# Kernel tuning notes

Hardware: AMD Instinct MI355X
Metric: run time of the kernel (lower is better)

Reference implementation:

```python
import jax, jax.numpy as jnp
import numpy as np
import math

SCALE = math.sqrt(256.0)

def setup_inputs() -> dict:
    key = jax.random.key(0)
    k1, k2, k3, k4, k5 = jax.random.split(key, 5)
    B, C, T, D = 8, 80, 2048, 256
    bound = 1.0 / math.sqrt(C)
    x = jax.random.normal(k1, (B, C, T), dtype=jnp.float32)
    Wk = jax.random.uniform(k2, (D, C), minval=-bound, maxval=bound, dtype=jnp.float32)
    bk = jax.random.uniform(k3, (D,), minval=-bound, maxval=bound, dtype=jnp.float32)
    Wq = jax.random.uniform(k4, (D, C), minval=-bound, maxval=bound, dtype=jnp.float32)
    bq = jax.random.uniform(k5, (D,), minval=-bound, maxval=bound, dtype=jnp.float32)
    return {"x": x, "Wk": Wk, "bk": bk, "Wq": Wq, "bq": bq}

def reference(x, Wk, bk, Wq, bq):
    # x: [B, C=80, T]; work in time-major layout [B, T, C]
    xt = jnp.swapaxes(x, 1, 2)                      # [B, T, C]
    K = xt @ Wk.T + bk                              # [B, T, 256]
    Q = xt @ Wq.T + bq                              # [B, T, 256]
    # softmax over last dim (dim=2 in torch) of K Q^T / sqrt(256)
    att = jax.nn.softmax(jnp.einsum('bid,bjd->bij', K, Q) / SCALE, axis=2)
    # original per-timestep loop is exactly att @ xt (values = raw input, no V proj)
    out = jnp.einsum('bij,bjc->bic', att, xt)       # [B, T, C]
    return jnp.swapaxes(out, 1, 2)                  # [B, C, T]
```

## Files before the change

kernel.cpp:

```cpp
#include <hip/hip_runtime.h>
#include <hip/hip_bf16.h>
#include <math.h>

typedef __bf16 bf16;
typedef __bf16 bf16x8 __attribute__((ext_vector_type(8)));
typedef float  f32x4  __attribute__((ext_vector_type(4)));
typedef float  f32x16 __attribute__((ext_vector_type(16)));
typedef uint32_t u32x4 __attribute__((ext_vector_type(4)));

#define MFMA16(a, b, c) __builtin_amdgcn_mfma_f32_16x16x32_bf16((a), (b), (c), 0, 0, 0)
#define MFMA32(a, b, c) __builtin_amdgcn_mfma_f32_32x32x16_bf16((a), (b), (c), 0, 0, 0)

typedef const uint32_t __attribute__((address_space(1)))* gq_t;
typedef uint32_t __attribute__((address_space(3)))* lq_t;

constexpr int B_ = 8, C_ = 80, T_ = 2048, D_ = 256;
constexpr int NS = 8;
constexpr float SCALE_INV = 1.0f / 16.0f;
constexpr float LOG2E_16 = 0.090169989f;

static __device__ inline uint32_t pkbf(float lo, float hi) {
  bf16 l = (bf16)lo, h = (bf16)hi;
  uint16_t lb = __builtin_bit_cast(uint16_t, l), hb = __builtin_bit_cast(uint16_t, h);
  return (uint32_t)lb | ((uint32_t)hb << 16);
}

__global__ __launch_bounds__(256) void proj_kernel(
    const float* __restrict__ x,
    const float* __restrict__ Wk,
    const float* __restrict__ bk,
    const float* __restrict__ Wq,
    const float* __restrict__ bq,
    bf16* __restrict__ Kb,
    bf16* __restrict__ Qb,
    bf16* __restrict__ xbf)
{
  const int t0   = blockIdx.x * 32;
  const int b    = blockIdx.y;
  const int tid  = threadIdx.x;
  const int w    = tid >> 6;
  const int lane = tid & 63;
  const int h    = lane >> 4;
  const int lr   = lane & 15;

  const float* xb = x + (size_t)b * C_ * T_;

  {
    bf16* ob = xbf + (size_t)b * C_ * T_;
    #pragma unroll
    for (int q = 0; q < 10; ++q) {
      int idx = q * 256 + tid;
      int c = idx >> 5, tt = idx & 31;
      ob[c * T_ + t0 + tt] = (bf16)xb[c * T_ + t0 + tt];
    }
  }

  bf16x8 afrag[2][3];
  #pragma unroll
  for (int ib = 0; ib < 2; ++ib) {
    int t = t0 + ib * 16 + lr;
    #pragma unroll
    for (int ks = 0; ks < 3; ++ks) {
      bf16x8 v;
      #pragma unroll
      for (int e = 0; e < 8; ++e) {
        int c = ks * 32 + h * 8 + e;
        float val;
        if (c < 80)       val = xb[c * T_ + t];
        else if (c == 80) val = 1.0f;
        else              val = 0.0f;
        v[e] = (bf16)val;
      }
      afrag[ib][ks] = v;
    }
  }

  const int nb0 = w * 4;
  #pragma unroll
  for (int mat = 0; mat < 2; ++mat) {
    const float* W    = mat ? Wq : Wk;
    const float* bias = mat ? bq : bk;
    bf16* outp        = mat ? Qb : Kb;

    f32x4 acc[2][4];
    #pragma unroll
    for (int ib = 0; ib < 2; ++ib)
      #pragma unroll
      for (int nb = 0; nb < 4; ++nb)
        acc[ib][nb] = f32x4{0.f, 0.f, 0.f, 0.f};

    #pragma unroll
    for (int nb = 0; nb < 4; ++nb) {
      int d = (nb0 + nb) * 16 + lr;
      #pragma unroll
      for (int ks = 0; ks < 3; ++ks) {
        bf16x8 bv;
        #pragma unroll
        for (int e = 0; e < 8; ++e) {
          int c = ks * 32 + h * 8 + e;
          float val;
          if (c < 80)       val = W[d * C_ + c];
          else if (c == 80) val = bias[d];
          else              val = 0.0f;
          bv[e] = (bf16)val;
        }
        #pragma unroll
        for (int ib = 0; ib < 2; ++ib)
          acc[ib][nb] = MFMA16(afrag[ib][ks], bv, acc[ib][nb]);
      }
    }

    #pragma unroll
    for (int ib = 0; ib < 2; ++ib)
      #pragma unroll
      for (int nb = 0; nb < 4; ++nb) {
        int d = (nb0 + nb) * 16 + lr;
        #pragma unroll
        for (int r = 0; r < 4; ++r) {
          int t = t0 + ib * 16 + h * 4 + r;
          outp[(size_t)(b * T_ + t) * D_ + d] = (bf16)acc[ib][nb][r];
        }
      }
  }
}

__global__ __launch_bounds__(256, 2) void attn_kernel(
    const bf16* __restrict__ Kb,
    const bf16* __restrict__ Qb,
    const bf16* __restrict__ xbf,
    float* __restrict__ Opart,
    float* __restrict__ mpart,
    float* __restrict__ lpart)
{
  constexpr int BN = 32, NT = T_ / BN;
  constexpr int JT_PER = NT / NS;
  __shared__ bf16 qlds[2][BN * D_];

  const int flat = blockIdx.x;
  const int b    = flat & 7;
  const int rem  = flat >> 3;
  const int it   = rem & 15;
  const int s    = rem >> 4;
  const int i0   = it * 128;

  const int tid  = threadIdx.x;
  const int w    = tid >> 6;
  const int lane = tid & 63;
  const int il   = lane & 31;
  const int hi   = lane >> 5;
  const int iw   = i0 + w * 32;

  const bf16* Kbase = Kb  + (size_t)b * T_ * D_;
  const bf16* Qbase = Qb  + (size_t)b * T_ * D_;
  const bf16* Vbase = xbf + (size_t)b * C_ * T_;

  bf16x8 kf[16];
  {
    const bf16* kp = Kbase + (size_t)(iw + il) * D_ + hi * 8;
    #pragma unroll
    for (int ks = 0; ks < 16; ++ks)
      kf[ks] = *reinterpret_cast<const bf16x8*>(kp + ks * 16);
  }

  f32x16 oacc[3];
  #pragma unroll
  for (int cb = 0; cb < 3; ++cb)
    #pragma unroll
    for (int r = 0; r < 16; ++r) oacc[cb][r] = 0.f;
  float m_run = -INFINITY, l_run = 0.f;

  auto stage = [&](int jt, int buf) {
    #pragma unroll
    for (int q = 0; q < 4; ++q) {
      int f = tid + 256 * q;
      int j = f >> 5, c = f & 31;
      const bf16* src = Qbase + (size_t)(jt * BN + j) * D_ + ((c ^ j) << 3);
      __builtin_amdgcn_global_load_lds((gq_t)src,
          (lq_t)&qlds[buf][(q * 256 + w * 64) * 8], 16, 0, 0);
    }
  };

  const int jt0 = s * JT_PER, jtend = jt0 + JT_PER;

  stage(jt0, 0);
  asm volatile("s_waitcnt vmcnt(0)" ::: "memory");
  __syncthreads();

  int cur = 0;
  for (int jt = jt0; jt < jtend; ++jt, cur ^= 1) {
    if (jt + 1 < jtend) stage(jt + 1, cur ^ 1);

    bf16x8 vf[3][2];
    #pragma unroll
    for (int cb = 0; cb < 3; ++cb)
      #pragma unroll
      for (int kj = 0; kj < 2; ++kj)
        vf[cb][kj] = *reinterpret_cast<const bf16x8*>(
            Vbase + (size_t)(cb * 32 + il) * T_ + jt * BN + hi * 8 + kj * 16);

    f32x16 sacc;
    #pragma unroll
    for (int r = 0; r < 16; ++r) sacc[r] = 0.f;
    __builtin_amdgcn_s_setprio(1);
    #pragma unroll
    for (int ks = 0; ks < 16; ++ks) {
      bf16x8 qa = *reinterpret_cast<const bf16x8*>(
          &qlds[cur][il * 256 + (((hi + 2 * ks) ^ il) << 3)]);
      sacc = MFMA32(qa, kf[ks], sacc);
    }
    __builtin_amdgcn_s_setprio(0);

    float p16[16];
    #pragma unroll
    for (int r = 0; r < 16; ++r) p16[r] = sacc[r];
    float mx = p16[0];
    #pragma unroll
    for (int r = 1; r < 16; ++r) mx = fmaxf(mx, p16[r]);
    mx = fmaxf(mx, __shfl_xor(mx, 32));

    if (!__all(mx <= m_run + 48.f)) {
      float mnew  = fmaxf(m_run, mx);
      float alpha = exp2f((m_run - mnew) * LOG2E_16);
      m_run = mnew;
      l_run *= alpha;
      #pragma unroll
      for (int cb = 0; cb < 3; ++cb)
        #pragma unroll
        for (int r = 0; r < 16; ++r) oacc[cb][r] *= alpha;
    }
    float rs = 0.f;
    #pragma unroll
    for (int r = 0; r < 16; ++r) {
      p16[r] = exp2f((p16[r] - m_run) * LOG2E_16);
      rs += p16[r];
    }
    rs += __shfl_xor(rs, 32);
    l_run += rs;

    uint32_t a0 = pkbf(p16[0],  p16[1]),  a1 = pkbf(p16[2],  p16[3]);
    uint32_t c0 = pkbf(p16[4],  p16[5]),  c1 = pkbf(p16[6],  p16[7]);
    uint32_t a2 = pkbf(p16[8],  p16[9]),  a3 = pkbf(p16[10], p16[11]);
    uint32_t c2 = pkbf(p16[12], p16[13]), c3 = pkbf(p16[14], p16[15]);
    uint32_t a0s = __shfl_xor(a0, 32), a1s = __shfl_xor(a1, 32);
    uint32_t c0s = __shfl_xor(c0, 32), c1s = __shfl_xor(c1, 32);
    uint32_t a2s = __shfl_xor(a2, 32), a3s = __shfl_xor(a3, 32);
    uint32_t c2s = __shfl_xor(c2, 32), c3s = __shfl_xor(c3, 32);
    const bool h = (hi != 0);
    u32x4 pb0 = { h ? c0s : a0, h ? c1s : a1, h ? c0 : a0s, h ? c1 : a1s };
    u32x4 pb1 = { h ? c2s : a2, h ? c3s : a3, h ? c2 : a2s, h ? c3 : a3s };
    bf16x8 pbf0 = __builtin_bit_cast(bf16x8, pb0);
    bf16x8 pbf1 = __builtin_bit_cast(bf16x8, pb1);

    __builtin_amdgcn_s_setprio(1);
    #pragma unroll
    for (int cb = 0; cb < 3; ++cb) {
      oacc[cb] = MFMA32(vf[cb][0], pbf0, oacc[cb]);
      oacc[cb] = MFMA32(vf[cb][1], pbf1, oacc[cb]);
    }
    __builtin_amdgcn_s_setprio(0);

    asm volatile("s_waitcnt vmcnt(0)" ::: "memory");
    __syncthreads();
  }

  float* ob = Opart + (size_t)(s * B_ + b) * C_ * T_;
  #pragma unroll
  for (int cb = 0; cb < 3; ++cb)
    #pragma unroll
    for (int r = 0; r < 16; ++r) {
      if (cb < 2 || r < 8) {
        int c = cb * 32 + (r & 3) + 8 * (r >> 2) + 4 * hi;
        ob[(size_t)c * T_ + iw + il] = oacc[cb][r];
      }
    }
  if (lane < 32) {
    mpart[(size_t)(s * B_ + b) * T_ + iw + il] = m_run;
    lpart[(size_t)(s * B_ + b) * T_ + iw + il] = l_run;
  }
}

__global__ __launch_bounds__(256) void merge_kernel(
    const float* __restrict__ Opart,
    const float* __restrict__ mpart,
    const float* __restrict__ lpart,
    float* __restrict__ out)
{
  const int b    = blockIdx.y;
  const int tid  = threadIdx.x;
  const int w    = tid >> 6;
  const int lane = tid & 63;
  const int t    = blockIdx.x * 64 + lane;

  float m[NS];
  float mmax = -INFINITY;
  #pragma unroll
  for (int s2 = 0; s2 < NS; ++s2) {
    m[s2] = mpart[(size_t)(s2 * B_ + b) * T_ + t];
    mmax = fmaxf(mmax, m[s2]);
  }
  float e[NS];
  float lsum = 0.f;
  #pragma unroll
  for (int s2 = 0; s2 < NS; ++s2) {
    e[s2] = exp2f((m[s2] - mmax) * LOG2E_16);
    lsum += e[s2] * lpart[(size_t)(s2 * B_ + b) * T_ + t];
  }
  const float inv = 1.0f / lsum;

  const int c0 = w * 20;
  for (int c = c0; c < c0 + 20; ++c) {
    float acc = 0.f;
    #pragma unroll
    for (int s2 = 0; s2 < NS; ++s2)
      acc += Opart[((size_t)(s2 * B_ + b) * C_ + c) * T_ + t] * e[s2];
    out[((size_t)b * C_ + c) * T_ + t] = acc * inv;
  }
}

extern "C" void kernel_launch(void* const* d_in, const int* in_sizes, int n_in,
                              void* d_out, int out_size, void* d_ws, size_t ws_size,
                              hipStream_t stream) {
  (void)in_sizes; (void)n_in; (void)out_size; (void)ws_size;
  const float* x  = (const float*)d_in[0];
  const float* Wk = (const float*)d_in[1];
  const float* bk = (const float*)d_in[2];
  const float* Wq = (const float*)d_in[3];
  const float* bq = (const float*)d_in[4];
  float* out = (float*)d_out;

  char* ws = (char*)d_ws;
  const size_t MB = 1024 * 1024;
  bf16*  Kb    = (bf16*)(ws);
  bf16*  Qb    = (bf16*)(ws + 8 * MB);
  bf16*  xbf   = (bf16*)(ws + 16 * MB);
  float* Opart = (float*)(ws + 19 * MB);
  float* mpart = (float*)(ws + 61 * MB);
  float* lpart = (float*)(ws + 62 * MB);

  dim3 blk(256);
  dim3 g1(T_ / 32, B_);
  proj_kernel<<<g1, blk, 0, stream>>>(x, Wk, bk, Wq, bq, Kb, Qb, xbf);
  attn_kernel<<<dim3(16 * NS * B_), blk, 0, stream>>>(Kb, Qb, xbf, Opart, mpart, lpart);
  dim3 g3(T_ / 64, B_);
  merge_kernel<<<g3, blk, 0, stream>>>(Opart, mpart, lpart, out);
}
```

Before: 76.61 us.

## Software-pipeline QK^T of next tile with softmax/PV and halve KV splits

Restructures the attention inner loop into a two-stage pipeline. The Q·K MFMAs and V loads for tile t+1 are issued before the softmax and P·V of tile t, with double-buffered score accumulators and V fragments, and LDS staging runs two tiles ahead. This is meant to hide the latency of the exp/shuffle softmax section behind matrix work. It also cuts the number of sequence splits from 8 to 4, which halves the partial outputs the merge kernel must read, and shrinks the workspace offsets to match. The cost is higher register pressure and half as many blocks for parallelism.

```diff
diff --git a/kernel.cpp b/kernel.cpp
--- a/kernel.cpp
+++ b/kernel.cpp
@@ -15,8 +15,7 @@
 typedef uint32_t __attribute__((address_space(3)))* lq_t;
 
 constexpr int B_ = 8, C_ = 80, T_ = 2048, D_ = 256;
-constexpr int NS = 8;
-constexpr float SCALE_INV = 1.0f / 16.0f;
+constexpr int NS = 4;
 constexpr float LOG2E_16 = 0.090169989f;
 
 static __device__ inline uint32_t pkbf(float lo, float hi) {
@@ -180,36 +179,29 @@
     }
   };
 
-  const int jt0 = s * JT_PER, jtend = jt0 + JT_PER;
-
-  stage(jt0, 0);
-  asm volatile("s_waitcnt vmcnt(0)" ::: "memory");
-  __syncthreads();
-
-  int cur = 0;
-  for (int jt = jt0; jt < jtend; ++jt, cur ^= 1) {
-    if (jt + 1 < jtend) stage(jt + 1, cur ^ 1);
-
-    bf16x8 vf[3][2];
+  auto vload = [&](int jt, bf16x8 (&vf)[3][2]) {
     #pragma unroll
     for (int cb = 0; cb < 3; ++cb)
       #pragma unroll
       for (int kj = 0; kj < 2; ++kj)
         vf[cb][kj] = *reinterpret_cast<const bf16x8*>(
             Vbase + (size_t)(cb * 32 + il) * T_ + jt * BN + hi * 8 + kj * 16);
-
-    f32x16 sacc;
-    #pragma unroll
-    for (int r = 0; r < 16; ++r) sacc[r] = 0.f;
+  };
+
+  auto qkt = [&](int buf, f32x16& sc) {
+    #pragma unroll
+    for (int r = 0; r < 16; ++r) sc[r] = 0.f;
     __builtin_amdgcn_s_setprio(1);
     #pragma unroll
     for (int ks = 0; ks < 16; ++ks) {
       bf16x8 qa = *reinterpret_cast<const bf16x8*>(
-          &qlds[cur][il * 256 + (((hi + 2 * ks) ^ il) << 3)]);
-      sacc = MFMA32(qa, kf[ks], sacc);
+          &qlds[buf][il * 256 + (((hi + 2 * ks) ^ il) << 3)]);
+      sc = MFMA32(qa, kf[ks], sc);
     }
     __builtin_amdgcn_s_setprio(0);
-
+  };
+
+  auto smax_pv = [&](f32x16& sacc, bf16x8 (&vf)[3][2]) {
     float p16[16];
     #pragma unroll
     for (int r = 0; r < 16; ++r) p16[r] = sacc[r];
@@ -245,9 +237,9 @@
     uint32_t c0s = __shfl_xor(c0, 32), c1s = __shfl_xor(c1, 32);
     uint32_t a2s = __shfl_xor(a2, 32), a3s = __shfl_xor(a3, 32);
     uint32_t c2s = __shfl_xor(c2, 32), c3s = __shfl_xor(c3, 32);
-    const bool h = (hi != 0);
-    u32x4 pb0 = { h ? c0s : a0, h ? c1s : a1, h ? c0 : a0s, h ? c1 : a1s };
-    u32x4 pb1 = { h ? c2s : a2, h ? c3s : a3, h ? c2 : a2s, h ? c3 : a3s };
+    const bool hh = (hi != 0);
+    u32x4 pb0 = { hh ? c0s : a0, hh ? c1s : a1, hh ? c0 : a0s, hh ? c1 : a1s };
+    u32x4 pb1 = { hh ? c2s : a2, hh ? c3s : a3, hh ? c2 : a2s, hh ? c3 : a3s };
     bf16x8 pbf0 = __builtin_bit_cast(bf16x8, pb0);
     bf16x8 pbf1 = __builtin_bit_cast(bf16x8, pb1);
 
@@ -258,9 +250,36 @@
       oacc[cb] = MFMA32(vf[cb][1], pbf1, oacc[cb]);
     }
     __builtin_amdgcn_s_setprio(0);
-
+  };
+
+  const int jt0 = s * JT_PER, jtend = jt0 + JT_PER;
+
+  f32x16 saccA, saccB;
+  bf16x8 vfA[3][2], vfB[3][2];
+
+  stage(jt0, 0);
+  asm volatile("s_waitcnt vmcnt(0)" ::: "memory");
+  __syncthreads();
+  vload(jt0, vfA);
+  qkt(0, saccA);
+  stage(jt0 + 1, 1);
+
+  auto body = [&](int t, f32x16& sp, f32x16& sc,
+                  bf16x8 (&va)[3][2], bf16x8 (&vb)[3][2], int par) {
     asm volatile("s_waitcnt vmcnt(0)" ::: "memory");
     __syncthreads();
+    if (t + 2 < jtend) stage(t + 2, par);
+    if (t + 1 < jtend) {
+      vload(t + 1, vb);
+      qkt(par ^ 1, sc);
+    }
+    smax_pv(sp, va);
+  };
+
+  #pragma unroll 1
+  for (int t = jt0; t < jtend; t += 2) {
+    body(t,     saccA, saccB, vfA, vfB, 0);
+    body(t + 1, saccB, saccA, vfB, vfA, 1);
   }
 
   float* ob = Opart + (size_t)(s * B_ + b) * C_ * T_;
@@ -334,8 +353,8 @@
   bf16*  Qb    = (bf16*)(ws + 8 * MB);
   bf16*  xbf   = (bf16*)(ws + 16 * MB);
   float* Opart = (float*)(ws + 19 * MB);
-  float* mpart = (float*)(ws + 61 * MB);
-  float* lpart = (float*)(ws + 62 * MB);
+  float* mpart = (float*)(ws + 41 * MB);
+  float* lpart = (float*)(ws + 42 * MB);
 
   dim3 blk(256);
   dim3 g1(T_ / 32, B_);
```

Result: slower. 115.5 us (+50.7%).
